# Performance work log

Measured on AMD Instinct MI355X. Metric: run time of the kernel, lower is better.

## Reference

```python
import jax, jax.numpy as jnp
import numpy as np

MARGIN = 0.3  # init_kwargs
EPS = 1e-12   # torch F.normalize eps


def _pairwise_dist(f):
    # Euclidean cdist via the stable quadratic expansion; f is [B, D].
    sq = jnp.sum(f * f, axis=1)                      # [B]
    d2 = sq[:, None] + sq[None, :] - 2.0 * (f @ f.T)  # [B, B]
    d2 = jnp.maximum(d2, 0.0)
    # safe sqrt: zero distance (diagonal / duplicates) -> 0 with zero grad
    pos = d2 > 0.0
    return jnp.sqrt(jnp.where(pos, d2, 1.0)) * pos


def reference(features, labels):
    B = features.shape[0]
    norm = jnp.linalg.norm(features, axis=1, keepdims=True)
    f = features / jnp.maximum(norm, EPS)            # F.normalize(dim=1)

    dist = _pairwise_dist(f)                         # [B, B]
    mask = labels[:, None] == labels[None, :]        # positives (incl. self)

    pos_count = jnp.sum(mask, axis=1)                # [B], >= 1 (self)
    has_pos = pos_count > 1                          # needs another positive
    has_neg = pos_count < B                          # at least one negative
    valid = has_pos & has_neg

    # mean over positive distances (includes the self-distance 0, as in torch code)
    mean_pos = jnp.sum(dist * mask, axis=1) / pos_count.astype(dist.dtype)  # [B]

    # semi-hard negatives: negatives with dist > mean positive dist
    sh_mask = (~mask) & (dist > mean_pos[:, None])   # [B, B]
    has_sh = jnp.any(sh_mask, axis=1)
    min_sh = jnp.min(jnp.where(sh_mask, dist, jnp.inf), axis=1)
    min_sh = jnp.where(has_sh, min_sh, 0.0)          # guard inf for invalid rows

    contrib = valid & has_sh
    per_anchor = jax.nn.relu(mean_pos - min_sh + MARGIN)
    loss_sum = jnp.sum(jnp.where(contrib, per_anchor, 0.0))
    count = jnp.sum(contrib)
    return jnp.where(count > 0, loss_sum / count.astype(dist.dtype), 0.0)


def setup_inputs() -> dict:
    key = jax.random.key(0)
    k1, k2 = jax.random.split(key)
    features = jax.random.normal(k1, (8192, 512), dtype=jnp.float32)
    labels = jax.random.randint(k2, (8192,), 0, 128, dtype=jnp.int64)
    return {"features": features, "labels": labels}
```

## Files before the change

### kernel.cpp

```cpp
#include <hip/hip_runtime.h>
#include <math.h>

#define EPS_N 1e-12f
#define MARGIN 0.3f
#define INF_BITS 0x7f800000u
#define NCLS 128
#define D 512
#define PADR 256

typedef __attribute__((ext_vector_type(8))) short short8;
typedef __attribute__((ext_vector_type(4))) float float4v;

__device__ __forceinline__ unsigned short f2bf(float f) {
    unsigned u = __float_as_uint(f);
    u += 0x7fff + ((u >> 16) & 1);
    return (unsigned short)(u >> 16);
}
__device__ __forceinline__ void gl16(const void* g, void* l) {
    __builtin_amdgcn_global_load_lds((const __attribute__((address_space(1))) void*)g,
                                     (__attribute__((address_space(3))) void*)l, 16, 0, 0);
}

__global__ __launch_bounds__(1024) void k_bucket(const int* __restrict__ lab, int Bn,
        int* __restrict__ pos, int* __restrict__ labp,
        int* __restrict__ cstart_g, int* __restrict__ ccnt_g,
        float* __restrict__ meanpos, float* __restrict__ pcinv,
        int* __restrict__ poscnt, unsigned* __restrict__ minbits) {
    __shared__ int cnt[NCLS], cs[NCLS + 1], off[NCLS], sa[NCLS], sb[NCLS];
    int tid = threadIdx.x;
    if (tid < NCLS) cnt[tid] = 0;
    __syncthreads();
    for (int i = tid; i < Bn; i += 1024) atomicAdd(&cnt[lab[i] & (NCLS - 1)], 1);
    __syncthreads();
    if (tid < NCLS) sa[tid] = cnt[tid];
    __syncthreads();
    int* src = sa; int* dst = sb;
    for (int ofs = 1; ofs < NCLS; ofs <<= 1) {
        if (tid < NCLS) dst[tid] = src[tid] + ((tid >= ofs) ? src[tid - ofs] : 0);
        __syncthreads();
        int* t = src; src = dst; dst = t;
    }
    if (tid < NCLS) {
        int ex = src[tid] - cnt[tid];
        cs[tid] = ex;
        off[tid] = ex;
        cstart_g[tid] = ex;
        ccnt_g[tid] = cnt[tid];
    }
    if (tid == 0) cs[NCLS] = Bn;
    __syncthreads();
    for (int p = tid; p < Bn; p += 1024) {
        int lo = 0, hi = NCLS - 1;
        #pragma unroll
        for (int s = 0; s < 7; ++s) {
            int mid = (lo + hi + 1) >> 1;
            if (cs[mid] <= p) lo = mid; else hi = mid - 1;
        }
        int l = lo, m = cnt[l];
        labp[p] = l;
        poscnt[p] = m;
        pcinv[p] = 1.0f / (float)m;
        meanpos[p] = 0.f;
        minbits[p] = INF_BITS;
    }
    for (int i = tid; i < Bn; i += 1024) {
        int l = lab[i] & (NCLS - 1);
        pos[i] = atomicAdd(&off[l], 1);
    }
}

__global__ __launch_bounds__(256) void k_normalize(const float* __restrict__ x,
        const int* __restrict__ pos, unsigned short* __restrict__ fh,
        float* __restrict__ sqp) {
    int w = threadIdx.x >> 6, L = threadIdx.x & 63;
    int row = blockIdx.x * 4 + w;
    const float* xr = x + (size_t)row * D + L * 8;
    float4 a = *(const float4*)xr;
    float4 b = *(const float4*)(xr + 4);
    float ss = a.x * a.x;
    ss = fmaf(a.y, a.y, ss); ss = fmaf(a.z, a.z, ss); ss = fmaf(a.w, a.w, ss);
    ss = fmaf(b.x, b.x, ss); ss = fmaf(b.y, b.y, ss);
    ss = fmaf(b.z, b.z, ss); ss = fmaf(b.w, b.w, ss);
    #pragma unroll
    for (int off = 32; off; off >>= 1) ss += __shfl_xor(ss, off, 64);
    float inv = 1.0f / fmaxf(sqrtf(ss), EPS_N);
    int prow = pos[row];
    if (L == 0) sqp[prow] = ss * inv * inv;
    ushort4 h0, h1;
    h0.x = f2bf(a.x * inv); h0.y = f2bf(a.y * inv);
    h0.z = f2bf(a.z * inv); h0.w = f2bf(a.w * inv);
    h1.x = f2bf(b.x * inv); h1.y = f2bf(b.y * inv);
    h1.z = f2bf(b.z * inv); h1.w = f2bf(b.w * inv);
    unsigned short* dst = fh + (size_t)prow * D + L * 8;
    *(ushort4*)dst = h0;
    *(ushort4*)(dst + 4) = h1;
}

__global__ __launch_bounds__(256) void k_posband3(
    const unsigned short* __restrict__ fh, const float* __restrict__ sqp,
    const int* __restrict__ labp, const int* __restrict__ cstart_g,
    const int* __restrict__ ccnt_g, float* __restrict__ meanpos, int Bn)
{
    __shared__ unsigned short SA[16 * 128];
    __shared__ unsigned short SB[128 * 128];
    __shared__ float sqr[16], rs[16];
    __shared__ int labr[16];
    __shared__ float sqc[128];
    __shared__ int labc[128];

    const int r0 = blockIdx.x * 16;
    const int tid = threadIdx.x, w = tid >> 6, L = tid & 63;
    const int lm = L & 15, ls = L >> 4;
    const int srow = L >> 4;
    const int sseg = L & 15;

    if (tid < 16) {
        labr[tid] = labp[r0 + tid];
        sqr[tid]  = sqp[r0 + tid];
        rs[tid]   = 0.f;
    }
    __syncthreads();
    const int c0 = cstart_g[labr[0]];
    const int c1 = cstart_g[labr[15]] + ccnt_g[labr[15]];

    for (int cc0 = c0; cc0 < c1; cc0 += 128) {
        __syncthreads();
        if (tid < 128) {
            int q = cc0 + tid;
            if (q < Bn) { sqc[tid] = sqp[q]; labc[tid] = labp[q]; }
            else        { sqc[tid] = 0.f;    labc[tid] = -1; }
        }
        float4v acc[2];
        acc[0] = (float4v){0.f, 0.f, 0.f, 0.f};
        acc[1] = (float4v){0.f, 0.f, 0.f, 0.f};

        for (int k0 = 0; k0 < D; k0 += 128) {
            __syncthreads();
            {
                int rmat = w * 4 + srow;
                int seg = sseg ^ (rmat & 15);
                gl16(fh + (size_t)(r0 + rmat) * D + k0 + seg * 8, &SA[(w * 4) * 128]);
            }
            #pragma unroll
            for (int it = 0; it < 8; ++it) {
                int rmat = it * 16 + w * 4 + srow;
                int seg = sseg ^ (rmat & 15);
                gl16(fh + (size_t)(cc0 + rmat) * D + k0 + seg * 8,
                     &SB[(size_t)(it * 16 + w * 4) * 128]);
            }
            __syncthreads();
            #pragma unroll
            for (int h = 0; h < 4; ++h) {
                int ra = lm;
                short8 af = *(const short8*)&SA[ra * 128 + (((h * 4 + ls) ^ (ra & 15))) * 8];
                #pragma unroll
                for (int ct = 0; ct < 2; ++ct) {
                    int rb = w * 32 + ct * 16 + lm;
                    short8 bf = *(const short8*)&SB[rb * 128 + (((h * 4 + ls) ^ (rb & 15))) * 8];
                    acc[ct] = __builtin_amdgcn_mfma_f32_16x16x32_bf16(af, bf, acc[ct], 0, 0, 0);
                }
            }
        }
        #pragma unroll
        for (int v = 0; v < 4; ++v) {
            int ri = ls * 4 + v;
            int p = r0 + ri;
            int lr = labr[ri];
            float sr = sqr[ri];
            float sum = 0.f;
            #pragma unroll
            for (int ct = 0; ct < 2; ++ct) {
                int ci = w * 32 + ct * 16 + lm;
                int q = cc0 + ci;
                float d2 = sr + sqc[ci] - 2.0f * acc[ct][v];
                float dd = (d2 > 0.f) ? sqrtf(d2) : 0.f;
                sum += ((labc[ci] == lr) && (q != p)) ? dd : 0.f;
            }
            #pragma unroll
            for (int off = 8; off; off >>= 1) sum += __shfl_xor(sum, off, 64);
            if (lm == 0) atomicAdd(&rs[ri], sum);
        }
    }
    __syncthreads();
    if (tid < 16 && rs[tid] != 0.f) atomicAdd(&meanpos[r0 + tid], rs[tid]);
}

#define NKT 8
#define BUFH 32768

__global__ __launch_bounds__(512, 2) void k_minsh_mfma(
    const unsigned short* __restrict__ fh, const float* __restrict__ sqp,
    const int* __restrict__ labp, const float* __restrict__ meanpos,
    const float* __restrict__ pcinv, unsigned* __restrict__ minbits)
{
    int t = (blockIdx.x & 7) * 66 + (blockIdx.x >> 3);
    int I = (int)((sqrtf(8.0f * (float)t + 1.0f) - 1.0f) * 0.5f);
    while ((I + 1) * (I + 2) / 2 <= t) ++I;
    while (I * (I + 1) / 2 > t) --I;
    const int J = t - I * (I + 1) / 2;
    const int i0 = I * 256, j0 = J * 256;

    __shared__ unsigned short LA[2][BUFH];
    __shared__ float s_mp2r[256], s_sqr[256], s_mp2c[256], s_sqc[256];
    __shared__ int s_labr[256], s_labc[256];

    const int tid = threadIdx.x;
    const int w = tid >> 6, L = tid & 63;
    const int lm = L & 15, ls = L >> 4;
    const int wm = w >> 2, wn = w & 3;
    const int u0 = ls ^ (lm & 7);
    const int u1 = (4 + ls) ^ (lm & 7);

    const unsigned short* srcA[4];
    const unsigned short* srcB[4];
    #pragma unroll
    for (int q = 0; q < 4; ++q) {
        int s = tid + 512 * q;
        int r = s >> 3;
        int u = (s & 7) ^ (r & 7);
        srcA[q] = fh + (size_t)(i0 + r) * D + u * 8;
        srcB[q] = fh + (size_t)(j0 + r) * D + u * 8;
    }

    #define K3_STAGE(kt_, b_) do {                                          \
        const int ko_ = (kt_) * 64;   \
        _Pragma("unroll")                                                   \
        for (int q = 0; q < 4; ++q)                                         \
            gl16(srcA[q] + ko_, &LA[(b_)][(w * 64 + 512 * q) * 8]);         \
        _Pragma("unroll")                                                   \
        for (int q = 0; q < 4; ++q)                                         \
            gl16(srcB[q] + ko_, &LA[(b_)][16384 + (w * 64 + 512 * q) * 8]); \
    } while (0)

    if (tid < 256) {
        int p = i0 + tid;
        float mp = meanpos[p] * pcinv[p];
        s_mp2r[tid] = mp * mp;
        s_sqr[tid]  = sqp[p];
        s_labr[tid] = labp[p];
    } else {
        int q = tid - 256, p = j0 + q;
        float mp = meanpos[p] * pcinv[p];
        s_mp2c[q] = mp * mp;
        s_sqc[q]  = sqp[p];
        s_labc[q] = labp[p];
    }

    float4v acc[8][4];
    #pragma unroll
    for (int mi = 0; mi < 8; ++mi)
        #pragma unroll
        for (int ni = 0; ni < 4; ++ni) acc[mi][ni] = (float4v){0.f, 0.f, 0.f, 0.f};

    K3_STAGE(0, 0);
    __builtin_amdgcn_sched_barrier(0);
    K3_STAGE(1, 1);
    asm volatile("s_waitcnt vmcnt(8)" ::: "memory");
    __builtin_amdgcn_sched_barrier(0);
    __builtin_amdgcn_s_barrier();
    __builtin_amdgcn_sched_barrier(0);

    const unsigned short* aB = &LA[0][(wm * 128 + lm) * 64];
    const unsigned short* bB = &LA[0][16384 + (wn * 64 + lm) * 64];

    for (int kt = 0; kt < NKT; ++kt) {
        const int co = (kt & 1) * BUFH;
        {
            short8 af[8], bf[4];
            #pragma unroll
            for (int mi = 0; mi < 8; ++mi)
                af[mi] = *(const short8*)(aB + co + mi * 1024 + u0 * 8);
            #pragma unroll
            for (int ni = 0; ni < 4; ++ni)
                bf[ni] = *(const short8*)(bB + co + ni * 1024 + u0 * 8);
            __builtin_amdgcn_s_setprio(1);
            #pragma unroll
            for (int ni = 0; ni < 4; ++ni)
                #pragma unroll
                for (int mi = 0; mi < 8; ++mi)
                    acc[mi][ni] = __builtin_amdgcn_mfma_f32_16x16x32_bf16(af[mi], bf[ni], acc[mi][ni], 0, 0, 0);
            __builtin_amdgcn_s_setprio(0);
        }
        {
            short8 af[8], bf[4];
            #pragma unroll
            for (int mi = 0; mi < 8; ++mi)
                af[mi] = *(const short8*)(aB + co + mi * 1024 + u1 * 8);
            #pragma unroll
            for (int ni = 0; ni < 4; ++ni)
                bf[ni] = *(const short8*)(bB + co + ni * 1024 + u1 * 8);
            asm volatile("s_waitcnt lgkmcnt(0)" ::: "memory");
            __builtin_amdgcn_sched_barrier(0);
            __builtin_amdgcn_s_barrier();
            __builtin_amdgcn_sched_barrier(0);
            if (kt + 2 < NKT) K3_STAGE(kt + 2, kt & 1);
            __builtin_amdgcn_s_setprio(1);
            #pragma unroll
            for (int ni = 0; ni < 4; ++ni)
                #pragma unroll
                for (int mi = 0; mi < 8; ++mi)
                    acc[mi][ni] = __builtin_amdgcn_mfma_f32_16x16x32_bf16(af[mi], bf[ni], acc[mi][ni], 0, 0, 0);
            __builtin_amdgcn_s_setprio(0);
        }
        if (kt + 1 < NKT) {
            if (kt + 2 < NKT) asm volatile("s_waitcnt vmcnt(8)" ::: "memory");
            else              asm volatile("s_waitcnt vmcnt(0)" ::: "memory");
            __builtin_amdgcn_sched_barrier(0);
            __builtin_amdgcn_s_barrier();
            __builtin_amdgcn_sched_barrier(0);
        }
    }
    #undef K3_STAGE

    unsigned* rminb = (unsigned*)&LA[0][0];
    unsigned* cminb = rminb + 256;
    __syncthreads();
    if (tid < 256) rminb[tid] = INF_BITS;
    else           cminb[tid - 256] = INF_BITS;
    __syncthreads();

    const float INFF = __uint_as_float(INF_BITS);
    float sc[4], mp2c[4]; int lc[4];
    #pragma unroll
    for (int ni = 0; ni < 4; ++ni) {
        int cl = wn * 64 + ni * 16 + lm;
        sc[ni]   = s_sqc[cl];
        mp2c[ni] = s_mp2c[cl];
        lc[ni]   = s_labc[cl];
    }
    float vminc[4];
    #pragma unroll
    for (int ni = 0; ni < 4; ++ni) vminc[ni] = INFF;

    #pragma unroll
    for (int mi = 0; mi < 8; ++mi) {
        #pragma unroll
        for (int v = 0; v < 4; ++v) {
            int rl = wm * 128 + mi * 16 + ls * 4 + v;
            float mp2r = s_mp2r[rl];
            float sr   = s_sqr[rl];
            int   li   = s_labr[rl];
            float vminr = INFF;
            #pragma unroll
            for (int ni = 0; ni < 4; ++ni) {
                float d2 = fmaf(-2.0f, acc[mi][ni][v], sr + sc[ni]);
                bool neq = (li != lc[ni]);
                vminr     = fminf(vminr,     (neq && d2 > mp2r)     ? d2 : INFF);
                vminc[ni] = fminf(vminc[ni], (neq && d2 > mp2c[ni]) ? d2 : INFF);
            }
            #pragma unroll
            for (int off = 8; off; off >>= 1)
                vminr = fminf(vminr, __shfl_xor(vminr, off, 64));
            if (lm == 0 && __float_as_uint(vminr) != INF_BITS)
                atomicMin(&rminb[rl], __float_as_uint(vminr));
        }
    }
    #pragma unroll
    for (int ni = 0; ni < 4; ++ni) {
        float vc = vminc[ni];
        vc = fminf(vc, __shfl_xor(vc, 16, 64));
        vc = fminf(vc, __shfl_xor(vc, 32, 64));
        if (ls == 0 && __float_as_uint(vc) != INF_BITS)
            atomicMin(&cminb[wn * 64 + ni * 16 + lm], __float_as_uint(vc));
    }
    __syncthreads();
    if (tid < 256) {
        unsigned rb = rminb[tid];
        if (rb != INF_BITS) atomicMin(&minbits[i0 + tid], rb);
    } else if (i0 != j0) {
        unsigned cb = cminb[tid - 256];
        if (cb != INF_BITS) atomicMin(&minbits[j0 + tid - 256], cb);
    }
}

__global__ __launch_bounds__(1024) void k_finish(const float* __restrict__ meanpos,
        const float* __restrict__ pcinv, const int* __restrict__ poscnt,
        const unsigned* __restrict__ minbits, float* __restrict__ out, int Bn) {
    float lsum = 0.f; int lcnt = 0;
    for (int i = threadIdx.x; i < Bn; i += 1024) {
        int pc = poscnt[i];
        bool valid = (pc > 1) && (pc < Bn);
        unsigned mb = minbits[i];
        if (valid && mb != INF_BITS) {
            float v = fmaf(meanpos[i], pcinv[i], MARGIN - sqrtf(__uint_as_float(mb)));
            lsum += (v > 0.f) ? v : 0.f;
            lcnt += 1;
        }
    }
    __shared__ float ssum[16]; __shared__ int scnt[16];
    int lane = threadIdx.x & 63, wid = threadIdx.x >> 6;
    #pragma unroll
    for (int off = 32; off; off >>= 1) {
        lsum += __shfl_down(lsum, off, 64);
        lcnt += __shfl_down(lcnt, off, 64);
    }
    if (lane == 0) { ssum[wid] = lsum; scnt[wid] = lcnt; }
    __syncthreads();
    if (threadIdx.x == 0) {
        float s = 0.f; int c = 0;
        #pragma unroll
        for (int q = 0; q < 16; ++q) { s += ssum[q]; c += scnt[q]; }
        out[0] = (c > 0) ? s / (float)c : 0.f;
    }
}

extern "C" void kernel_launch(void* const* d_in, const int* in_sizes, int n_in,
                              void* d_out, int out_size, void* d_ws, size_t ws_size,
                              hipStream_t stream) {
    const float* x = (const float*)d_in[0];
    const int* lab = (const int*)d_in[1];
    int Bn = in_sizes[1];

    size_t nd = (size_t)(Bn + PADR) * D;
    unsigned short* fh = (unsigned short*)d_ws;
    float* sqp        = (float*)(fh + nd);
    float* meanpos    = sqp + Bn;
    float* pcinv      = meanpos + Bn;
    int* poscnt       = (int*)(pcinv + Bn);
    unsigned* minbits = (unsigned*)(poscnt + Bn);
    int* pos          = (int*)(minbits + Bn);
    int* labp         = pos + Bn;
    int* cstart_g     = labp + Bn;
    int* ccnt_g       = cstart_g + NCLS;

    k_bucket<<<1, 1024, 0, stream>>>(lab, Bn, pos, labp, cstart_g, ccnt_g,
                                     meanpos, pcinv, poscnt, minbits);
    k_normalize<<<Bn / 4, 256, 0, stream>>>(x, pos, fh, sqp);
    k_posband3<<<Bn / 16, 256, 0, stream>>>(fh, sqp, labp, cstart_g, ccnt_g,
                                            meanpos, Bn);
    int nbr = Bn / 256;
    int T = nbr * (nbr + 1) / 2;
    k_minsh_mfma<<<T, 512, 0, stream>>>(fh, sqp, labp, meanpos, pcinv, minbits);
    k_finish<<<1, 1024, 0, stream>>>(meanpos, pcinv, poscnt, minbits,
                                     (float*)d_out, Bn);
}
```

Baseline: 173.3 us.

## Interleave quarter-tile global-to-LDS prefetch with MFMA sub-groups in minsh GEMM loop

Restructures the main GEMM loop of the semi-hard-negative kernel so the next tile's global_load_lds copies are split into four quarter stages, each issued between smaller 16-MFMA sub-groups. Register fragment loads drop from 12 to 8 per sub-step, and the loop is fully unrolled with tighter vmcnt waits. The aim is to spread memory issue across the compute instead of bursting it at one barrier, and to reduce register pressure. The cost is a more intricate schedule whose wait counts must exactly match the number of outstanding loads.

```diff
diff --git a/kernel.cpp b/kernel.cpp
--- a/kernel.cpp
+++ b/kernel.cpp
@@ -200,7 +200,7 @@
     const int J = t - I * (I + 1) / 2;
     const int i0 = I * 256, j0 = J * 256;
 
-    __shared__ unsigned short LA[2][BUFH];
+    __shared__ unsigned short LA[2 * BUFH];
     __shared__ float s_mp2r[256], s_sqr[256], s_mp2c[256], s_sqc[256];
     __shared__ int s_labr[256], s_labc[256];
 
@@ -209,7 +209,7 @@
     const int lm = L & 15, ls = L >> 4;
     const int wm = w >> 2, wn = w & 3;
     const int u0 = ls ^ (lm & 7);
-    const int u1 = (4 + ls) ^ (lm & 7);
+    const int u1 = u0 ^ 4;
 
     const unsigned short* srcA[4];
     const unsigned short* srcB[4];
@@ -221,16 +221,71 @@
         srcA[q] = fh + (size_t)(i0 + r) * D + u * 8;
         srcB[q] = fh + (size_t)(j0 + r) * D + u * 8;
     }
-
-    #define K3_STAGE(kt_, b_) do {                                          \
-        const int ko_ = (kt_) * 64;   \
-        _Pragma("unroll")                                                   \
-        for (int q = 0; q < 4; ++q)                                         \
-            gl16(srcA[q] + ko_, &LA[(b_)][(w * 64 + 512 * q) * 8]);         \
-        _Pragma("unroll")                                                   \
-        for (int q = 0; q < 4; ++q)                                         \
-            gl16(srcB[q] + ko_, &LA[(b_)][16384 + (w * 64 + 512 * q) * 8]); \
-    } while (0)
+    unsigned short* LAm = &LA[0];
+    const unsigned short* aB = LAm + (wm * 128 + lm) * 64;
+    const unsigned short* bB = LAm + 16384 + (wn * 64 + lm) * 64;
+
+#define STAGE_HF(t_, hf_) do {                                               \
+    int ko_ = (t_) * 64;                                                     \
+    unsigned short* db_ = LAm + ((t_) & 1) * BUFH + (((hf_) >= 2) ? 16384 : 0); \
+    const unsigned short* const* sp_ = ((hf_) >= 2) ? srcB : srcA;           \
+    int q0_ = ((hf_) & 1) * 2;                                               \
+    gl16(sp_[q0_] + ko_,     db_ + (w * 64 + 512 * q0_) * 8);                \
+    gl16(sp_[q0_ + 1] + ko_, db_ + (w * 64 + 512 * (q0_ + 1)) * 8);          \
+} while (0)
+
+#define MM16(mlo_)                                                           \
+    __builtin_amdgcn_s_setprio(1);                                           \
+    _Pragma("unroll")                                                        \
+    for (int ni = 0; ni < 4; ++ni) {                                         \
+        _Pragma("unroll")                                                    \
+        for (int k = 0; k < 4; ++k)                                          \
+            acc[(mlo_) + k][ni] = __builtin_amdgcn_mfma_f32_16x16x32_bf16(   \
+                af[k], bf[ni], acc[(mlo_) + k][ni], 0, 0, 0);                 \
+    }                                                                        \
+    __builtin_amdgcn_s_setprio(0);
+
+#define GROUP(co_, g_, DO1_, DO0_, WAITK_) do {                              \
+    short8 af[4], bf[4];                                                     \
+                                                                     \
+    _Pragma("unroll")                                                        \
+    for (int ni = 0; ni < 4; ++ni) bf[ni] = *(const short8*)(bB + (co_) + ni * 1024 + u0 * 8); \
+    _Pragma("unroll")                                                        \
+    for (int k = 0; k < 4; ++k)  af[k] = *(const short8*)(aB + (co_) + k * 1024 + u0 * 8); \
+    if (DO1_) STAGE_HF((g_) + 1, 1);                                         \
+    MM16(0);                                                                 \
+    __builtin_amdgcn_sched_barrier(0);                                       \
+                                                                     \
+    _Pragma("unroll")                                                        \
+    for (int k = 0; k < 4; ++k)  af[k] = *(const short8*)(aB + (co_) + (4 + k) * 1024 + u0 * 8); \
+    if (DO1_) STAGE_HF((g_) + 1, 2);                                         \
+    MM16(4);                                                                 \
+    __builtin_amdgcn_sched_barrier(0);                                       \
+                                                                     \
+    _Pragma("unroll")                                                        \
+    for (int ni = 0; ni < 4; ++ni) bf[ni] = *(const short8*)(bB + (co_) + ni * 1024 + u1 * 8); \
+    _Pragma("unroll")                                                        \
+    for (int k = 0; k < 4; ++k)  af[k] = *(const short8*)(aB + (co_) + k * 1024 + u1 * 8); \
+    if (DO1_) STAGE_HF((g_) + 1, 3);                                         \
+    MM16(0);                                                                 \
+    __builtin_amdgcn_sched_barrier(0);                                       \
+                                                                     \
+    _Pragma("unroll")                                                        \
+    for (int k = 0; k < 4; ++k)  af[k] = *(const short8*)(aB + (co_) + (4 + k) * 1024 + u1 * 8); \
+    asm volatile("s_waitcnt lgkmcnt(0)" ::: "memory");                       \
+    __builtin_amdgcn_sched_barrier(0);                                       \
+    __builtin_amdgcn_s_barrier();           \
+    __builtin_amdgcn_sched_barrier(0);                                       \
+    if (DO0_) STAGE_HF((g_) + 2, 0);                                         \
+    MM16(4);                                                                 \
+    if ((WAITK_) == 2)      { asm volatile("s_waitcnt vmcnt(2)" ::: "memory"); } \
+    else if ((WAITK_) == 0) { asm volatile("s_waitcnt vmcnt(0)" ::: "memory"); } \
+    __builtin_amdgcn_sched_barrier(0);                                       \
+    if ((WAITK_) >= 0) {                                                     \
+        __builtin_amdgcn_s_barrier();        \
+        __builtin_amdgcn_sched_barrier(0);                                   \
+    }                                                                        \
+} while (0)
 
     if (tid < 256) {
         int p = i0 + tid;
@@ -245,6 +300,7 @@
         s_sqc[q]  = sqp[p];
         s_labc[q] = labp[p];
     }
+    __builtin_amdgcn_sched_barrier(0);
 
     float4v acc[8][4];
     #pragma unroll
@@ -252,67 +308,26 @@
         #pragma unroll
         for (int ni = 0; ni < 4; ++ni) acc[mi][ni] = (float4v){0.f, 0.f, 0.f, 0.f};
 
-    K3_STAGE(0, 0);
-    __builtin_amdgcn_sched_barrier(0);
-    K3_STAGE(1, 1);
-    asm volatile("s_waitcnt vmcnt(8)" ::: "memory");
+    STAGE_HF(0, 0); STAGE_HF(0, 1); STAGE_HF(0, 2); STAGE_HF(0, 3);
+    STAGE_HF(1, 0);
+    asm volatile("s_waitcnt vmcnt(2)" ::: "memory");
     __builtin_amdgcn_sched_barrier(0);
     __builtin_amdgcn_s_barrier();
     __builtin_amdgcn_sched_barrier(0);
 
-    const unsigned short* aB = &LA[0][(wm * 128 + lm) * 64];
-    const unsigned short* bB = &LA[0][16384 + (wn * 64 + lm) * 64];
-
-    for (int kt = 0; kt < NKT; ++kt) {
-        const int co = (kt & 1) * BUFH;
-        {
-            short8 af[8], bf[4];
-            #pragma unroll
-            for (int mi = 0; mi < 8; ++mi)
-                af[mi] = *(const short8*)(aB + co + mi * 1024 + u0 * 8);
-            #pragma unroll
-            for (int ni = 0; ni < 4; ++ni)
-                bf[ni] = *(const short8*)(bB + co + ni * 1024 + u0 * 8);
-            __builtin_amdgcn_s_setprio(1);
-            #pragma unroll
-            for (int ni = 0; ni < 4; ++ni)
-                #pragma unroll
-                for (int mi = 0; mi < 8; ++mi)
-                    acc[mi][ni] = __builtin_amdgcn_mfma_f32_16x16x32_bf16(af[mi], bf[ni], acc[mi][ni], 0, 0, 0);
-            __builtin_amdgcn_s_setprio(0);
-        }
-        {
-            short8 af[8], bf[4];
-            #pragma unroll
-            for (int mi = 0; mi < 8; ++mi)
-                af[mi] = *(const short8*)(aB + co + mi * 1024 + u1 * 8);
-            #pragma unroll
-            for (int ni = 0; ni < 4; ++ni)
-                bf[ni] = *(const short8*)(bB + co + ni * 1024 + u1 * 8);
-            asm volatile("s_waitcnt lgkmcnt(0)" ::: "memory");
-            __builtin_amdgcn_sched_barrier(0);
-            __builtin_amdgcn_s_barrier();
-            __builtin_amdgcn_sched_barrier(0);
-            if (kt + 2 < NKT) K3_STAGE(kt + 2, kt & 1);
-            __builtin_amdgcn_s_setprio(1);
-            #pragma unroll
-            for (int ni = 0; ni < 4; ++ni)
-                #pragma unroll
-                for (int mi = 0; mi < 8; ++mi)
-                    acc[mi][ni] = __builtin_amdgcn_mfma_f32_16x16x32_bf16(af[mi], bf[ni], acc[mi][ni], 0, 0, 0);
-            __builtin_amdgcn_s_setprio(0);
-        }
-        if (kt + 1 < NKT) {
-            if (kt + 2 < NKT) asm volatile("s_waitcnt vmcnt(8)" ::: "memory");
-            else              asm volatile("s_waitcnt vmcnt(0)" ::: "memory");
-            __builtin_amdgcn_sched_barrier(0);
-            __builtin_amdgcn_s_barrier();
-            __builtin_amdgcn_sched_barrier(0);
-        }
-    }
-    #undef K3_STAGE
-
-    unsigned* rminb = (unsigned*)&LA[0][0];
+    #pragma unroll
+    for (int g = 0; g < NKT - 2; ++g) {
+        const int co = (g & 1) * BUFH;
+        GROUP(co, g, true, true, 2);
+    }
+    GROUP(((NKT - 2) & 1) * BUFH, NKT - 2, true,  false, 0);
+    GROUP(((NKT - 1) & 1) * BUFH, NKT - 1, false, false, -1);
+
+#undef GROUP
+#undef MM16
+#undef STAGE_HF
+
+    unsigned* rminb = (unsigned*)&LA[0];
     unsigned* cminb = rminb + 256;
     __syncthreads();
     if (tid < 256) rminb[tid] = INF_BITS;
```

After: 177.7 us. 1.03x slower.
